# Optimization experiments

Hardware: AMD Instinct MI355X
Metric: run time of the kernel (lower is better)

Reference implementation:

```python
import jax, jax.numpy as jnp
import numpy as np

B, F, C, H, W = 256, 16, 256, 32, 32

def setup_inputs() -> dict:
    key = jax.random.key(0)
    kx, kk = jax.random.split(key)
    x = jax.random.normal(kx, (B, C, H, W), dtype=jnp.float32)
    # kaiming_normal init: std = sqrt(2 / fan_in), fan_in = C*H*W
    std = float(np.sqrt(2.0 / (C * H * W)))
    kernel = jax.random.normal(kk, (F, C, H, W), dtype=jnp.float32) * std
    return {"x": x, "kernel": kernel}

def reference(x, kernel):
    # (x[:,None] * kernel[None]).sum((-1,-2)) == einsum over spatial dims, per channel
    y = jnp.einsum('bchw,fchw->bfc', x, kernel)  # [B, F, C]
    return y.reshape(y.shape[0], -1)  # [B, F*C]
```

## Files before the change

kernel.cpp:

```cpp
#include <hip/hip_runtime.h>
#include <hip/hip_bf16.h>


constexpr int Bb = 256;
constexpr int Ff = 16;
constexpr int Cc = 256;
constexpr int HW = 1024;
constexpr int CHW = Cc * HW;

constexpr int BT = 128;
constexpr int RB = 4;
constexpr int NTHREADS = (BT / RB) * 16;
constexpr int NJ = HW / 4 / 16;

__device__ __forceinline__ float dot4(float4 a, float4 b) {
    return a.x * b.x + a.y * b.y + a.z * b.z + a.w * b.w;
}
__device__ __forceinline__ float red16(float v) {
    v += __shfl_xor(v, 1);
    v += __shfl_xor(v, 2);
    v += __shfl_xor(v, 4);
    v += __shfl_xor(v, 8);
    return v;
}

__global__ __launch_bounds__(NTHREADS)
void sle_kernel(const float* __restrict__ x, const float* __restrict__ k,
                float* __restrict__ out) {
    __shared__ float ldsK[Ff * HW];

    const int t   = threadIdx.x;
    const int thw = t & 15;
    const int tbg = t >> 4;

    const int g     = blockIdx.x;
    const int c     = (g & 7) * 32 + ((g >> 3) & 31);
    const int btile = g >> 8;
    const int b0    = btile * BT + tbg * RB;

    {
        const int fr = t >> 5, lane32 = t & 31;
        const float4* src = (const float4*)(k + (size_t)fr * CHW + (size_t)c * HW);
        float4* dst = (float4*)(ldsK + fr * HW);
#pragma unroll
        for (int q = 0; q < 8; ++q)
            dst[lane32 + 32 * q] = src[lane32 + 32 * q];
    }
    __syncthreads();

    const float* xb = x + (size_t)c * HW;
    const int xo0 = (b0 + 0) * CHW;
    const int xo1 = (b0 + 1) * CHW;
    const int xo2 = (b0 + 2) * CHW;
    const int xo3 = (b0 + 3) * CHW;

    float4 a00={0,0,0,0}, a01={0,0,0,0}, a02={0,0,0,0}, a03={0,0,0,0};
    float4 a10={0,0,0,0}, a11={0,0,0,0}, a12={0,0,0,0}, a13={0,0,0,0};
    float4 a20={0,0,0,0}, a21={0,0,0,0}, a22={0,0,0,0}, a23={0,0,0,0};
    float4 a30={0,0,0,0}, a31={0,0,0,0}, a32={0,0,0,0}, a33={0,0,0,0};

#pragma unroll 2
    for (int j = 0; j < NJ; ++j) {
        const int off = 4 * (thw + 16 * j);
        const float4 xv0 = *(const float4*)(xb + xo0 + off);
        const float4 xv1 = *(const float4*)(xb + xo1 + off);
        const float4 xv2 = *(const float4*)(xb + xo2 + off);
        const float4 xv3 = *(const float4*)(xb + xo3 + off);

#define ACC_G(G, A0, A1, A2, A3) {                                      \
        const float* kp = ldsK + (4 * (G)) * HW + off;                  \
        const float4 k0 = *(const float4*)(kp);                         \
        const float4 k1 = *(const float4*)(kp + HW);                    \
        const float4 k2 = *(const float4*)(kp + 2 * HW);                \
        const float4 k3 = *(const float4*)(kp + 3 * HW);                \
        A0.x += dot4(xv0, k0); A0.y += dot4(xv0, k1);                   \
        A0.z += dot4(xv0, k2); A0.w += dot4(xv0, k3);                   \
        A1.x += dot4(xv1, k0); A1.y += dot4(xv1, k1);                   \
        A1.z += dot4(xv1, k2); A1.w += dot4(xv1, k3);                   \
        A2.x += dot4(xv2, k0); A2.y += dot4(xv2, k1);                   \
        A2.z += dot4(xv2, k2); A2.w += dot4(xv2, k3);                   \
        A3.x += dot4(xv3, k0); A3.y += dot4(xv3, k1);                   \
        A3.z += dot4(xv3, k2); A3.w += dot4(xv3, k3); }

        ACC_G(0, a00, a10, a20, a30)
        ACC_G(1, a01, a11, a21, a31)
        ACC_G(2, a02, a12, a22, a32)
        ACC_G(3, a03, a13, a23, a33)
#undef ACC_G
    }

#define RED4(A) { A.x = red16(A.x); A.y = red16(A.y); \
                  A.z = red16(A.z); A.w = red16(A.w); }
    RED4(a00) RED4(a01) RED4(a02) RED4(a03)
    RED4(a10) RED4(a11) RED4(a12) RED4(a13)
    RED4(a20) RED4(a21) RED4(a22) RED4(a23)
    RED4(a30) RED4(a31) RED4(a32) RED4(a33)
#undef RED4

    __syncthreads();
    if (thw == 0) {
        float4* r0 = (float4*)(ldsK + (tbg * RB + 0) * Ff);
        float4* r1 = (float4*)(ldsK + (tbg * RB + 1) * Ff);
        float4* r2 = (float4*)(ldsK + (tbg * RB + 2) * Ff);
        float4* r3 = (float4*)(ldsK + (tbg * RB + 3) * Ff);
        r0[0] = a00; r0[1] = a01; r0[2] = a02; r0[3] = a03;
        r1[0] = a10; r1[1] = a11; r1[2] = a12; r1[3] = a13;
        r2[0] = a20; r2[1] = a21; r2[2] = a22; r2[3] = a23;
        r3[0] = a30; r3[1] = a31; r3[2] = a32; r3[3] = a33;
    }
    __syncthreads();

#pragma unroll
    for (int i = 0; i < (BT * Ff) / NTHREADS; ++i) {
        const int idx = t + NTHREADS * i;
        const int bl  = idx >> 4;
        const int f   = idx & 15;
        out[(size_t)(btile * BT + bl) * (Ff * Cc) + f * Cc + c] = ldsK[idx];
    }
}

extern "C" void kernel_launch(void* const* d_in, const int* in_sizes, int n_in,
                              void* d_out, int out_size, void* d_ws, size_t ws_size,
                              hipStream_t stream) {
    const float* x = (const float*)d_in[0];
    const float* k = (const float*)d_in[1];
    float* out = (float*)d_out;
    const int grid = Cc * (Bb / BT);
    sle_kernel<<<grid, NTHREADS, 0, stream>>>(x, k, out);
}
```

Baseline: 390.4 us.

## Write results coalesced to workspace and transpose in a separate kernel

The main kernel now stores each block's results contiguously into a workspace laid out channel-major, replacing scattered stride-C stores to the output. A second LDS-tiled transpose kernel then rearranges the workspace into the required [B, F*C] layout with coalesced float4 accesses. This removes uncoalesced global writes in exchange for an extra kernel launch and an additional round trip of the output through memory. The original path is kept as a fallback when the workspace is too small.

```diff
diff --git a/kernel.cpp b/kernel.cpp
--- a/kernel.cpp
+++ b/kernel.cpp
@@ -24,9 +24,10 @@
     return v;
 }
 
+template <bool TO_WS>
 __global__ __launch_bounds__(NTHREADS)
 void sle_kernel(const float* __restrict__ x, const float* __restrict__ k,
-                float* __restrict__ out) {
+                float* __restrict__ dst) {
     __shared__ float ldsK[Ff * HW];
 
     const int t   = threadIdx.x;
@@ -41,10 +42,10 @@
     {
         const int fr = t >> 5, lane32 = t & 31;
         const float4* src = (const float4*)(k + (size_t)fr * CHW + (size_t)c * HW);
-        float4* dst = (float4*)(ldsK + fr * HW);
+        float4* dstk = (float4*)(ldsK + fr * HW);
 #pragma unroll
         for (int q = 0; q < 8; ++q)
-            dst[lane32 + 32 * q] = src[lane32 + 32 * q];
+            dstk[lane32 + 32 * q] = src[lane32 + 32 * q];
     }
     __syncthreads();
 
@@ -110,12 +111,50 @@
     }
     __syncthreads();
 
+    if (TO_WS) {
+        float4 v = *(const float4*)(ldsK + 4 * t);
+        *(float4*)(dst + (size_t)c * (Bb * Ff) + btile * (BT * Ff) + 4 * t) = v;
+    } else {
 #pragma unroll
-    for (int i = 0; i < (BT * Ff) / NTHREADS; ++i) {
-        const int idx = t + NTHREADS * i;
-        const int bl  = idx >> 4;
-        const int f   = idx & 15;
-        out[(size_t)(btile * BT + bl) * (Ff * Cc) + f * Cc + c] = ldsK[idx];
+        for (int i = 0; i < (BT * Ff) / NTHREADS; ++i) {
+            const int idx = t + NTHREADS * i;
+            const int bl  = idx >> 4;
+            const int f   = idx & 15;
+            dst[(size_t)(btile * BT + bl) * (Ff * Cc) + f * Cc + c] = ldsK[idx];
+        }
+    }
+}
+
+constexpr int TS = 64;
+__global__ __launch_bounds__(256)
+void trans_kernel(const float* __restrict__ yT, float* __restrict__ out) {
+    __shared__ float tl[TS][TS + 1];
+    const int t  = threadIdx.x;
+    const int bi = blockIdx.x & 63;
+    const int bj = blockIdx.x >> 6;
+    const int r0 = bi * TS, c0 = bj * TS;
+    const int rr = t & 15, cl = t >> 4;
+
+#pragma unroll
+    for (int q = 0; q < 4; ++q) {
+        const int c_local = cl + 16 * q;
+        const float4 v = *(const float4*)(yT + (size_t)(c0 + c_local) * 4096
+                                              + r0 + 4 * rr);
+        tl[c_local][4 * rr + 0] = v.x;
+        tl[c_local][4 * rr + 1] = v.y;
+        tl[c_local][4 * rr + 2] = v.z;
+        tl[c_local][4 * rr + 3] = v.w;
+    }
+    __syncthreads();
+#pragma unroll
+    for (int q = 0; q < 4; ++q) {
+        const int r_local = cl + 16 * q;
+        float4 v;
+        v.x = tl[4 * rr + 0][r_local];
+        v.y = tl[4 * rr + 1][r_local];
+        v.z = tl[4 * rr + 2][r_local];
+        v.w = tl[4 * rr + 3][r_local];
+        *(float4*)(out + (size_t)(r0 + r_local) * 256 + c0 + 4 * rr) = v;
     }
 }
 
@@ -126,5 +165,12 @@
     const float* k = (const float*)d_in[1];
     float* out = (float*)d_out;
     const int grid = Cc * (Bb / BT);
-    sle_kernel<<<grid, NTHREADS, 0, stream>>>(x, k, out);
+    const size_t need = (size_t)Cc * Bb * Ff * sizeof(float);
+    if (ws_size >= need && d_ws != nullptr) {
+        float* yT = (float*)d_ws;
+        sle_kernel<true><<<grid, NTHREADS, 0, stream>>>(x, k, yT);
+        trans_kernel<<<256, 256, 0, stream>>>(yT, out);
+    } else {
+        sle_kernel<false><<<grid, NTHREADS, 0, stream>>>(x, k, out);
+    }
 }
```

Result: no change. 391.5 us (+0.3%).
